# Kernel optimization log

Measured on AMD Instinct MI355X. Metric: run time of the kernel, lower is better.

## Reference

```python
import jax, jax.numpy as jnp
import numpy as np

B, N, E = 4, 2048, 1024
A, H = 64, 16          # attention_feature_dim, heads
D = A                   # per-head dim per source's rearrange quirk: d = attention_feature_dim
DK = A / H              # source scales by sqrt(attention_feature_dim / heads) = sqrt(4)
NEG_INF = jnp.float32(-jnp.inf)


def setup_inputs() -> dict:
    key = jax.random.key(0)
    ks = jax.random.split(key, 6)
    x = jax.random.normal(ks[0], (B, N, E), dtype=jnp.float32)
    mask = jax.random.randint(ks[1], (B, N), 0, 2, dtype=jnp.int32)
    # nn.Linear(E, A*H*3): weight [out,in] -> store transposed [in,out] for x @ W
    w_qkv = jax.random.normal(ks[2], (E, A * H * 3), dtype=jnp.float32) / np.sqrt(E)
    b_qkv = jax.random.normal(ks[3], (A * H * 3,), dtype=jnp.float32) * 0.02
    w_out = jax.random.normal(ks[4], (A * H, E), dtype=jnp.float32) / np.sqrt(A * H)
    b_out = jax.random.normal(ks[5], (E,), dtype=jnp.float32) * 0.02
    return {"x": x, "mask": mask, "w_qkv": w_qkv, "b_qkv": b_qkv,
            "w_out": w_out, "b_out": b_out}


def reference(x, mask, w_qkv, b_qkv, w_out, b_out):
    b, n, _ = x.shape
    qkv = x @ w_qkv + b_qkv                         # [b, n, 3*H*D]
    q, k, v = jnp.split(qkv, 3, axis=-1)            # each [b, n, H*D]
    def to_heads(t):
        return t.reshape(b, n, H, D).transpose(0, 2, 1, 3)  # [b, H, n, D]
    q, k, v = to_heads(q), to_heads(k), to_heads(v)
    scale = jnp.float32(1.0 / np.sqrt(DK))
    scores = jnp.einsum('bhqd,bhkd->bhqk', q, k) * scale    # [b, H, n, n]
    # mask: [b, n] -> [b, 1, 1, n]; masked positions (==0) get -inf
    scores = jnp.where(mask[:, None, None, :] == 0, NEG_INF, scores)
    attn = jax.nn.softmax(scores, axis=-1)
    out = jnp.einsum('bhqk,bhkd->bhqd', attn, v)            # [b, H, n, D]
    out = out.transpose(0, 2, 1, 3).reshape(b, n, H * D)    # [b, n, H*D]
    return out @ w_out + b_out                              # [b, n, E]
```

## Files before the change

kernel.cpp:

```cpp
#include <hip/hip_runtime.h>


typedef __bf16 bf16;
typedef __attribute__((ext_vector_type(8))) __bf16 bf16x8;
typedef __attribute__((ext_vector_type(4))) float f32x4;

#define MFMA16(a, b, c) __builtin_amdgcn_mfma_f32_16x16x32_bf16(a, b, c, 0, 0, 0)
#define GLOAD_LDS(src, dst) __builtin_amdgcn_global_load_lds( \
    (const __attribute__((address_space(1))) void*)(src),     \
    (__attribute__((address_space(3))) void*)(dst), 16, 0, 0)
#define BAR() __builtin_amdgcn_s_barrier()
#define VMCNT(n) asm volatile("s_waitcnt vmcnt(" #n ")" ::: "memory")

#define QSCALE 0.72134752f

__global__ __launch_bounds__(256, 1) void cvt_f32_bf16(
    const float* __restrict__ in, bf16* __restrict__ out, int n4)
{
    int i = blockIdx.x * 256 + threadIdx.x;
    if (i >= n4) return;
    float4 v = *(const float4*)(in + (size_t)i * 4);
    union { ushort4 u; bf16 h[4]; } o;
    o.h[0] = (bf16)v.x; o.h[1] = (bf16)v.y; o.h[2] = (bf16)v.z; o.h[3] = (bf16)v.w;
    *(ushort4*)(out + (size_t)i * 4) = o.u;
}

__global__ __launch_bounds__(256, 1) void transpose_f32_bf16(
    const float* __restrict__ in, bf16* __restrict__ out, int R, int C,
    int scale_rows, float scale)
{
    __shared__ float s[64][65];
    const int t  = threadIdx.x;
    const int r0 = blockIdx.y * 64;
    const int c0 = blockIdx.x * 64;
    const int tr  = t >> 4;
    const int tc4 = (t & 15) * 4;
#pragma unroll
    for (int p = 0; p < 4; ++p) {
        int r = tr + p * 16;
        float4 v = *(const float4*)(in + (size_t)(r0 + r) * C + c0 + tc4);
        s[r][tc4 + 0] = v.x; s[r][tc4 + 1] = v.y;
        s[r][tc4 + 2] = v.z; s[r][tc4 + 3] = v.w;
    }
    __syncthreads();
    const int cw  = t >> 3;
    const int rw8 = (t & 7) * 8;
#pragma unroll
    for (int p = 0; p < 2; ++p) {
        int c = cw + p * 32;
        float f = (c0 + c) < scale_rows ? scale : 1.0f;
        union { uint4 v; bf16 h[8]; } u;
#pragma unroll
        for (int j = 0; j < 8; ++j) u.h[j] = (bf16)(s[rw8 + j][c] * f);
        *(uint4*)(out + (size_t)(c0 + c) * R + r0 + rw8) = u.v;
    }
}

template <typename OutT>
__global__ __launch_bounds__(512, 2) void gemm128x256_kernel(
    const bf16* __restrict__ A, const bf16* __restrict__ Bt,
    const float* __restrict__ bias, OutT* __restrict__ C,
    int M, int N, int K, int qcols, float qscale, int nbx)
{
    __shared__ __align__(16) bf16 As[3 * 128 * 64];
    __shared__ __align__(16) bf16 Bs[3 * 256 * 64];

    const int t    = threadIdx.x;
    const int lane = t & 63;
    const int wave = t >> 6;
    const int wr   = wave >> 2;
    const int wc   = wave & 3;
    const int l15  = lane & 15;
    const int g    = lane >> 4;

    const int nwg = gridDim.x;
    const int cpx = nwg >> 3;
    const int wg  = blockIdx.x;
    const int swz = (wg & 7) * cpx + (wg >> 3);
    const int m0  = (swz / nbx) * 128;
    const int n0  = (swz % nbx) * 256;

    const int ntile = K >> 6;

    int srow[2], sblk[2];
#pragma unroll
    for (int r = 0; r < 2; ++r) {
        int s = t * 16 + r * 8192;
        srow[r] = s >> 7;
        int blk = (s >> 4) & 7;
        sblk[r] = blk ^ (srow[r] & 7);
    }
    const int ldst0 = t * 8;

    const bf16* Abase = A  + (size_t)m0 * K;
    const bf16* Bbase = Bt + (size_t)n0 * K;

    const f32x4 z = {0.f, 0.f, 0.f, 0.f};
    f32x4 acc[4][4];
#pragma unroll
    for (int i = 0; i < 4; ++i)
#pragma unroll
        for (int j = 0; j < 4; ++j) acc[i][j] = z;

    auto stageA = [&](int tile, int slot) {
        if (tile >= ntile) return;
        bf16* dst = As + slot * 8192;
        const bf16* src = Abase + tile * 64;
#pragma unroll
        for (int r = 0; r < 2; ++r)
            GLOAD_LDS(src + (size_t)srow[r] * K + sblk[r] * 8,
                      dst + ldst0 + r * 4096);
    };
    auto stageBh = [&](int tile, int slot, int h) {
        if (tile >= ntile) return;
        bf16* dst = Bs + slot * 16384 + h * 8192;
        const bf16* src = Bbase + (size_t)(h * 128) * K + tile * 64;
#pragma unroll
        for (int r = 0; r < 2; ++r)
            GLOAD_LDS(src + (size_t)srow[r] * K + sblk[r] * 8,
                      dst + ldst0 + r * 4096);
    };

#define LOAD_AF(slot)                                                         \
    _Pragma("unroll")                                                         \
    for (int f = 0; f < 4; ++f) {                                             \
        int row = wr * 64 + f * 16 + l15;                                     \
        _Pragma("unroll")                                                     \
        for (int ks = 0; ks < 2; ++ks)                                        \
            af[f][ks] = *(const bf16x8*)(&As[(slot) * 8192 + row * 64 +       \
                            (((ks * 4 + g) ^ (row & 7)) * 8)]);               \
    }
#define LOAD_BF(slot, half, dstv)                                             \
    _Pragma("unroll")                                                         \
    for (int c2 = 0; c2 < 2; ++c2) {                                          \
        int row = wc * 64 + ((half) * 2 + c2) * 16 + l15;                     \
        _Pragma("unroll")                                                     \
        for (int ks = 0; ks < 2; ++ks)                                        \
            dstv[c2][ks] = *(const bf16x8*)(&Bs[(slot) * 16384 + row * 64 +   \
                            (((ks * 4 + g) ^ (row & 7)) * 8)]);               \
    }
#define MFMA_H(bv, half)                                                      \
    {                                                                         \
        __builtin_amdgcn_s_setprio(1);                                        \
        _Pragma("unroll")                                                     \
        for (int f = 0; f < 4; ++f)                                           \
            _Pragma("unroll")                                                 \
            for (int c2 = 0; c2 < 2; ++c2) {                                  \
                acc[f][(half) * 2 + c2] = MFMA16(                             \
                    af[f][0], bv[c2][0], acc[f][(half) * 2 + c2]);            \
                acc[f][(half) * 2 + c2] = MFMA16(                             \
                    af[f][1], bv[c2][1], acc[f][(half) * 2 + c2]);            \
            }                                                                 \
        __builtin_amdgcn_s_setprio(0);                                        \
    }

    stageA(0, 0); stageBh(0, 0, 0); stageBh(0, 0, 1);
    stageA(1, 1); stageBh(1, 1, 0); stageBh(1, 1, 1);
    VMCNT(6);
    BAR();

    int slot = 0;
    for (int T = 0; T < ntile; ++T) {
        int slot2 = slot + 2; if (slot2 >= 3) slot2 -= 3;
        bf16x8 af[4][2], blo[2][2], bhi[2][2];
        LOAD_AF(slot);
        LOAD_BF(slot, 0, blo);
        stageA(T + 2, slot2);
        stageBh(T + 2, slot2, 0);
        MFMA_H(blo, 0);
        BAR();
        LOAD_BF(slot, 1, bhi);
        stageBh(T + 2, slot2, 1);
        MFMA_H(bhi, 1);
        if (T + 1 < ntile) {
            if (T + 2 < ntile) { VMCNT(6); } else { VMCNT(0); }
        }
        BAR();
        slot = (slot == 2) ? 0 : slot + 1;
    }

#undef LOAD_AF
#undef LOAD_BF
#undef MFMA_H

#pragma unroll
    for (int f = 0; f < 4; ++f) {
        int row = m0 + wr * 64 + f * 16 + g * 4;
#pragma unroll
        for (int cf = 0; cf < 4; ++cf) {
            int col = n0 + wc * 64 + cf * 16 + l15;
            float bs = bias[col];
            if (col < qcols) bs *= qscale;
#pragma unroll
            for (int r = 0; r < 4; ++r) {
                float v = acc[f][cf][r] + bs;
                C[(size_t)(row + r) * N + col] = (OutT)v;
            }
        }
    }
}

__global__ __launch_bounds__(256, 1) void vtrans_kernel(
    const bf16* __restrict__ qkv, bf16* __restrict__ vtg)
{
    __shared__ float tile[64][65];
    const int t  = threadIdx.x;
    const int n0 = blockIdx.x * 64;
    const int bh = blockIdx.y;
    const int b  = bh >> 4, h = bh & 15;
    const bf16* src = qkv + (size_t)(b * 2048 + n0) * 3072 + 2048 + h * 64;
#pragma unroll
    for (int r = 0; r < 2; ++r) {
        int s = t + r * 256;
        int row = s >> 3, c8 = (s & 7) * 8;
        union { uint4 v; bf16 h8[8]; } u;
        u.v = *(const uint4*)(src + (size_t)row * 3072 + c8);
#pragma unroll
        for (int j = 0; j < 8; ++j) tile[row][c8 + j] = (float)u.h8[j];
    }
    __syncthreads();
    bf16* dst = vtg + (size_t)bh * (64 * 2048) + n0;
#pragma unroll
    for (int r = 0; r < 2; ++r) {
        int s = t + r * 256;
        int d = s >> 3, n8 = (s & 7) * 8;
        union { uint4 v; bf16 h8[8]; } o;
#pragma unroll
        for (int j = 0; j < 8; ++j) o.h8[j] = (bf16)tile[n8 + j][d];
        *(uint4*)(dst + (size_t)d * 2048 + n8) = o.v;
    }
}

__global__ __launch_bounds__(256, 3) void attn_kernel(
    const bf16* __restrict__ qkv, const bf16* __restrict__ vtg,
    const int* __restrict__ mask, bf16* __restrict__ O)
{
    __shared__ __align__(16) bf16 Ks[2][64 * 64];
    __shared__ __align__(16) bf16 Vt[2][64 * 64];
    __shared__ __align__(16) bf16 Ps[4][16 * 88];
    __shared__ float mneg[2048];

    const int t    = threadIdx.x;
    const int lane = t & 63;
    const int wave = t >> 6;
    const int l15  = lane & 15;
    const int g    = lane >> 4;

    const int bid = (blockIdx.x & 7) * 128 + (blockIdx.x >> 3);
    const int qt  = bid & 15;
    const int bh  = bid >> 4;
    const int h   = bh & 15;
    const int b   = bh >> 4;
    const int q0  = qt * 128 + wave * 16;

    const int* mrow = mask + b * 2048;
    for (int i = t; i < 2048; i += 256)
        mneg[i] = mrow[i] ? 0.0f : -1e30f;

    const size_t RS = 3072;
    const bf16* qp0 = qkv + (size_t)(b * 2048 + q0 + l15) * RS + h * 64 + g * 8;
    const bf16* qp1 = qp0 + (size_t)64 * RS;
    bf16x8 aQ[2][2];
    aQ[0][0] = *(const bf16x8*)(qp0);
    aQ[0][1] = *(const bf16x8*)(qp0 + 32);
    aQ[1][0] = *(const bf16x8*)(qp1);
    aQ[1][1] = *(const bf16x8*)(qp1 + 32);

    const bf16* kbase = qkv + (size_t)(b * 2048) * RS + 1024 + h * 64;
    const bf16* vbase = vtg + (size_t)bh * (64 * 2048);

    const int e0 = t * 8;
    int srow[2], scol[2];
#pragma unroll
    for (int r = 0; r < 2; ++r) {
        int e   = e0 + r * 2048;
        int row = e >> 6;
        int cb  = (e >> 3) & 7;
        srow[r] = row;
        scol[r] = ((cb ^ (row & 7)) * 8);
    }

    const int rb0 = ((g)     ^ (l15 & 7)) * 8;
    const int rb1 = ((4 + g) ^ (l15 & 7)) * 8;

    const f32x4 z = {0.f, 0.f, 0.f, 0.f};
    f32x4 o0[4] = {z, z, z, z}, o1[4] = {z, z, z, z};
    f32x4 lacc0 = z, lacc1 = z;

    bf16x8 ones;
#pragma unroll
    for (int j = 0; j < 8; ++j) ones[j] = (bf16)1.0f;

#pragma unroll
    for (int r = 0; r < 2; ++r) {
        GLOAD_LDS(kbase + (size_t)srow[r] * RS + scol[r],   &Ks[0][e0 + r * 2048]);
        GLOAD_LDS(vbase + (size_t)srow[r] * 2048 + scol[r], &Vt[0][e0 + r * 2048]);
    }
    asm volatile("s_waitcnt vmcnt(0)" ::: "memory");
    __syncthreads();

    for (int i = 0; i < 32; ++i) {
        const int kc  = i * 64;
        const int buf = i & 1;

        if (i + 1 < 32) {
#pragma unroll
            for (int r = 0; r < 2; ++r) {
                GLOAD_LDS(kbase + (size_t)(kc + 64 + srow[r]) * RS + scol[r],
                          &Ks[buf ^ 1][e0 + r * 2048]);
                GLOAD_LDS(vbase + (size_t)srow[r] * 2048 + kc + 64 + scol[r],
                          &Vt[buf ^ 1][e0 + r * 2048]);
            }
        }

        float mb[4];
#pragma unroll
        for (int kt = 0; kt < 4; ++kt) mb[kt] = mneg[kc + kt * 16 + l15];

        bf16x8 bk[4][2];
#pragma unroll
        for (int kt = 0; kt < 4; ++kt) {
            const bf16* kr = &Ks[buf][(kt * 16 + l15) * 64];
            bk[kt][0] = *(const bf16x8*)(kr + rb0);
            bk[kt][1] = *(const bf16x8*)(kr + rb1);
        }

        f32x4 S[4];
#pragma unroll
        for (int kt = 0; kt < 4; ++kt) {
            f32x4 ini = {mb[kt], mb[kt], mb[kt], mb[kt]};
            S[kt] = MFMA16(aQ[0][0], bk[kt][0], ini);
            S[kt] = MFMA16(aQ[0][1], bk[kt][1], S[kt]);
        }
#pragma unroll
        for (int kt = 0; kt < 4; ++kt)
#pragma unroll
            for (int r = 0; r < 4; ++r)
                Ps[wave][(g * 4 + r) * 88 + kt * 16 + l15] =
                    (bf16)__builtin_amdgcn_exp2f(S[kt][r]);
        asm volatile("s_waitcnt lgkmcnt(0)" ::: "memory");
        const bf16x8 aP00 = *(const bf16x8*)(&Ps[wave][l15 * 88 + g * 8]);
        const bf16x8 aP01 = *(const bf16x8*)(&Ps[wave][l15 * 88 + 32 + g * 8]);
        asm volatile("s_waitcnt lgkmcnt(0)" ::: "memory");

#pragma unroll
        for (int kt = 0; kt < 4; ++kt) {
            f32x4 ini = {mb[kt], mb[kt], mb[kt], mb[kt]};
            S[kt] = MFMA16(aQ[1][0], bk[kt][0], ini);
            S[kt] = MFMA16(aQ[1][1], bk[kt][1], S[kt]);
        }

        bf16x8 bv[4][2];
#pragma unroll
        for (int dt = 0; dt < 4; ++dt) {
            const bf16* vr = &Vt[buf][(dt * 16 + l15) * 64];
            bv[dt][0] = *(const bf16x8*)(vr + rb0);
            bv[dt][1] = *(const bf16x8*)(vr + rb1);
        }

#pragma unroll
        for (int kt = 0; kt < 4; ++kt)
#pragma unroll
            for (int r = 0; r < 4; ++r)
                Ps[wave][(g * 4 + r) * 88 + kt * 16 + l15] =
                    (bf16)__builtin_amdgcn_exp2f(S[kt][r]);

        lacc0 = MFMA16(aP00, ones, lacc0);
        lacc0 = MFMA16(aP01, ones, lacc0);
#pragma unroll
        for (int dt = 0; dt < 4; ++dt) {
            o0[dt] = MFMA16(aP00, bv[dt][0], o0[dt]);
            o0[dt] = MFMA16(aP01, bv[dt][1], o0[dt]);
        }
        asm volatile("s_waitcnt lgkmcnt(0)" ::: "memory");
        const bf16x8 aP10 = *(const bf16x8*)(&Ps[wave][l15 * 88 + g * 8]);
        const bf16x8 aP11 = *(const bf16x8*)(&Ps[wave][l15 * 88 + 32 + g * 8]);

        lacc1 = MFMA16(aP10, ones, lacc1);
        lacc1 = MFMA16(aP11, ones, lacc1);
#pragma unroll
        for (int dt = 0; dt < 4; ++dt) {
            o1[dt] = MFMA16(aP10, bv[dt][0], o1[dt]);
            o1[dt] = MFMA16(aP11, bv[dt][1], o1[dt]);
        }

        asm volatile("s_waitcnt vmcnt(0)" ::: "memory");
        __syncthreads();
    }

    float inv0[4], inv1[4];
#pragma unroll
    for (int r = 0; r < 4; ++r) {
        inv0[r] = 1.0f / fmaxf(lacc0[r], 1e-30f);
        inv1[r] = 1.0f / fmaxf(lacc1[r], 1e-30f);
    }
#pragma unroll
    for (int nt = 0; nt < 4; ++nt) {
#pragma unroll
        for (int r = 0; r < 4; ++r) {
            int d = nt * 16 + l15;
            int row0 = q0 + g * 4 + r;
            O[(size_t)(b * 2048 + row0) * 1024 + h * 64 + d] = (bf16)(o0[nt][r] * inv0[r]);
            O[(size_t)(b * 2048 + row0 + 64) * 1024 + h * 64 + d] = (bf16)(o1[nt][r] * inv1[r]);
        }
    }
}

extern "C" void kernel_launch(void* const* d_in, const int* in_sizes, int n_in,
                              void* d_out, int out_size, void* d_ws, size_t ws_size,
                              hipStream_t stream)
{
    const float* x     = (const float*)d_in[0];
    const int*   mask  = (const int*)d_in[1];
    const float* w_qkv = (const float*)d_in[2];
    const float* b_qkv = (const float*)d_in[3];
    const float* w_out = (const float*)d_in[4];
    const float* b_out = (const float*)d_in[5];
    float* out = (float*)d_out;

    char* ws = (char*)d_ws;
    bf16* qkvb  = (bf16*)(ws);
    bf16* Obuf  = (bf16*)(ws + 50331648);
    bf16* xb    = (bf16*)(ws + 67108864);
    bf16* wqkvT = (bf16*)(ws + 83886080);
    bf16* woutT = (bf16*)(ws + 90177536);
    bf16* vtg   = xb;

    cvt_f32_bf16<<<dim3(8192), 256, 0, stream>>>(x, xb, 2097152);
    transpose_f32_bf16<<<dim3(48, 16), 256, 0, stream>>>(w_qkv, wqkvT, 1024, 3072,
                                                         1024, QSCALE);
    transpose_f32_bf16<<<dim3(16, 16), 256, 0, stream>>>(w_out, woutT, 1024, 1024,
                                                         0, 1.0f);
    gemm128x256_kernel<bf16><<<dim3(768), 512, 0, stream>>>(
        xb, wqkvT, b_qkv, qkvb, 8192, 3072, 1024, 1024, QSCALE, 12);
    vtrans_kernel<<<dim3(32, 64), 256, 0, stream>>>(qkvb, vtg);
    attn_kernel<<<dim3(1024), 256, 0, stream>>>(qkvb, vtg, mask, Obuf);
    gemm128x256_kernel<float><<<dim3(256), 512, 0, stream>>>(
        Obuf, woutT, b_out, out, 8192, 1024, 1024, 0, 1.0f, 4);
}
```

Before: 302.6 us.

## Compute transposed scores so P stays in registers, dropping the LDS round trip

Swaps the MFMA operand order so S^T comes out in a layout that can feed straight into the PV MFMA as the B operand. This removes the per-wave Ps shared-memory staging buffer and its waits. The row-sum MFMAs against a ones vector are replaced with scalar accumulation plus cross-lane swizzle and bpermute reductions at the end. V fragments are now read with split 8-byte LDS loads to match the new layout, and output stores are vectorized to 4 bf16 per store. The risks are more VGPR pressure, since both S tiles stay live, and more scalar adds in the softmax loop.

```diff
diff --git a/kernel.cpp b/kernel.cpp
--- a/kernel.cpp
+++ b/kernel.cpp
@@ -237,8 +237,7 @@
 {
     __shared__ __align__(16) bf16 Ks[2][64 * 64];
     __shared__ __align__(16) bf16 Vt[2][64 * 64];
-    __shared__ __align__(16) bf16 Ps[4][16 * 88];
-    __shared__ float mneg[2048];
+    __shared__ __align__(16) float mneg[2048];
 
     const int t    = threadIdx.x;
     const int lane = t & 63;
@@ -285,11 +284,7 @@
 
     const f32x4 z = {0.f, 0.f, 0.f, 0.f};
     f32x4 o0[4] = {z, z, z, z}, o1[4] = {z, z, z, z};
-    f32x4 lacc0 = z, lacc1 = z;
-
-    bf16x8 ones;
-#pragma unroll
-    for (int j = 0; j < 8; ++j) ones[j] = (bf16)1.0f;
+    float dsum0 = 0.0f, dsum1 = 0.0f;
 
 #pragma unroll
     for (int r = 0; r < 2; ++r) {
@@ -313,96 +308,80 @@
             }
         }
 
-        float mb[4];
-#pragma unroll
-        for (int kt = 0; kt < 4; ++kt) mb[kt] = mneg[kc + kt * 16 + l15];
-
-        bf16x8 bk[4][2];
+        f32x4 S0[4], S1[4];
 #pragma unroll
         for (int kt = 0; kt < 4; ++kt) {
+            f32x4 mq;
+#pragma unroll
+            for (int r = 0; r < 4; ++r)
+                mq[r] = mneg[kc + kt * 16 + g * 4 + r];
             const bf16* kr = &Ks[buf][(kt * 16 + l15) * 64];
-            bk[kt][0] = *(const bf16x8*)(kr + rb0);
-            bk[kt][1] = *(const bf16x8*)(kr + rb1);
-        }
-
-        f32x4 S[4];
-#pragma unroll
-        for (int kt = 0; kt < 4; ++kt) {
-            f32x4 ini = {mb[kt], mb[kt], mb[kt], mb[kt]};
-            S[kt] = MFMA16(aQ[0][0], bk[kt][0], ini);
-            S[kt] = MFMA16(aQ[0][1], bk[kt][1], S[kt]);
-        }
-#pragma unroll
-        for (int kt = 0; kt < 4; ++kt)
-#pragma unroll
-            for (int r = 0; r < 4; ++r)
-                Ps[wave][(g * 4 + r) * 88 + kt * 16 + l15] =
-                    (bf16)__builtin_amdgcn_exp2f(S[kt][r]);
-        asm volatile("s_waitcnt lgkmcnt(0)" ::: "memory");
-        const bf16x8 aP00 = *(const bf16x8*)(&Ps[wave][l15 * 88 + g * 8]);
-        const bf16x8 aP01 = *(const bf16x8*)(&Ps[wave][l15 * 88 + 32 + g * 8]);
-        asm volatile("s_waitcnt lgkmcnt(0)" ::: "memory");
-
-#pragma unroll
-        for (int kt = 0; kt < 4; ++kt) {
-            f32x4 ini = {mb[kt], mb[kt], mb[kt], mb[kt]};
-            S[kt] = MFMA16(aQ[1][0], bk[kt][0], ini);
-            S[kt] = MFMA16(aQ[1][1], bk[kt][1], S[kt]);
-        }
-
-        bf16x8 bv[4][2];
+            bf16x8 bk0 = *(const bf16x8*)(kr + rb0);
+            bf16x8 bk1 = *(const bf16x8*)(kr + rb1);
+            S0[kt] = MFMA16(bk0, aQ[0][0], mq);
+            S0[kt] = MFMA16(bk1, aQ[0][1], S0[kt]);
+            S1[kt] = MFMA16(bk0, aQ[1][0], mq);
+            S1[kt] = MFMA16(bk1, aQ[1][1], S1[kt]);
+        }
+
+        bf16x8 pb0[2], pb1[2];
+#pragma unroll
+        for (int m = 0; m < 2; ++m) {
+            union { bf16 hh[8]; bf16x8 v; } a, c;
+#pragma unroll
+            for (int kk = 0; kk < 2; ++kk) {
+#pragma unroll
+                for (int r = 0; r < 4; ++r) {
+                    float e0f = __builtin_amdgcn_exp2f(S0[2 * m + kk][r]);
+                    float e1f = __builtin_amdgcn_exp2f(S1[2 * m + kk][r]);
+                    a.hh[kk * 4 + r] = (bf16)e0f;
+                    c.hh[kk * 4 + r] = (bf16)e1f;
+                    dsum0 += e0f;
+                    dsum1 += e1f;
+                }
+            }
+            pb0[m] = a.v;
+            pb1[m] = c.v;
+        }
+
 #pragma unroll
         for (int dt = 0; dt < 4; ++dt) {
             const bf16* vr = &Vt[buf][(dt * 16 + l15) * 64];
-            bv[dt][0] = *(const bf16x8*)(vr + rb0);
-            bv[dt][1] = *(const bf16x8*)(vr + rb1);
-        }
-
-#pragma unroll
-        for (int kt = 0; kt < 4; ++kt)
-#pragma unroll
-            for (int r = 0; r < 4; ++r)
-                Ps[wave][(g * 4 + r) * 88 + kt * 16 + l15] =
-                    (bf16)__builtin_amdgcn_exp2f(S[kt][r]);
-
-        lacc0 = MFMA16(aP00, ones, lacc0);
-        lacc0 = MFMA16(aP01, ones, lacc0);
-#pragma unroll
-        for (int dt = 0; dt < 4; ++dt) {
-            o0[dt] = MFMA16(aP00, bv[dt][0], o0[dt]);
-            o0[dt] = MFMA16(aP01, bv[dt][1], o0[dt]);
-        }
-        asm volatile("s_waitcnt lgkmcnt(0)" ::: "memory");
-        const bf16x8 aP10 = *(const bf16x8*)(&Ps[wave][l15 * 88 + g * 8]);
-        const bf16x8 aP11 = *(const bf16x8*)(&Ps[wave][l15 * 88 + 32 + g * 8]);
-
-        lacc1 = MFMA16(aP10, ones, lacc1);
-        lacc1 = MFMA16(aP11, ones, lacc1);
-#pragma unroll
-        for (int dt = 0; dt < 4; ++dt) {
-            o1[dt] = MFMA16(aP10, bv[dt][0], o1[dt]);
-            o1[dt] = MFMA16(aP11, bv[dt][1], o1[dt]);
+            const int s7 = l15 & 7;
+#pragma unroll
+            for (int m = 0; m < 2; ++m) {
+                union { uint2 d2[2]; bf16x8 v; } vv;
+                vv.d2[0] = *(const uint2*)(vr + (((4 * m     + (g >> 1)) ^ s7) * 8) + (g & 1) * 4);
+                vv.d2[1] = *(const uint2*)(vr + (((4 * m + 2 + (g >> 1)) ^ s7) * 8) + (g & 1) * 4);
+                o0[dt] = MFMA16(vv.v, pb0[m], o0[dt]);
+                o1[dt] = MFMA16(vv.v, pb1[m], o1[dt]);
+            }
         }
 
         asm volatile("s_waitcnt vmcnt(0)" ::: "memory");
         __syncthreads();
     }
 
-    float inv0[4], inv1[4];
-#pragma unroll
-    for (int r = 0; r < 4; ++r) {
-        inv0[r] = 1.0f / fmaxf(lacc0[r], 1e-30f);
-        inv1[r] = 1.0f / fmaxf(lacc1[r], 1e-30f);
-    }
-#pragma unroll
-    for (int nt = 0; nt < 4; ++nt) {
+    dsum0 += __int_as_float(__builtin_amdgcn_ds_swizzle(__float_as_int(dsum0), 0x401F));
+    dsum1 += __int_as_float(__builtin_amdgcn_ds_swizzle(__float_as_int(dsum1), 0x401F));
+    const int swap32 = (lane ^ 32) << 2;
+    dsum0 += __int_as_float(__builtin_amdgcn_ds_bpermute(swap32, __float_as_int(dsum0)));
+    dsum1 += __int_as_float(__builtin_amdgcn_ds_bpermute(swap32, __float_as_int(dsum1)));
+    const float inv0 = 1.0f / fmaxf(dsum0, 1e-30f);
+    const float inv1 = 1.0f / fmaxf(dsum1, 1e-30f);
+
+    bf16* op0 = O + (size_t)(b * 2048 + q0 + l15) * 1024 + h * 64 + g * 4;
+    bf16* op1 = op0 + (size_t)64 * 1024;
+#pragma unroll
+    for (int dt = 0; dt < 4; ++dt) {
+        union { bf16 hh[4]; ushort4 u; } s0, s1;
 #pragma unroll
         for (int r = 0; r < 4; ++r) {
-            int d = nt * 16 + l15;
-            int row0 = q0 + g * 4 + r;
-            O[(size_t)(b * 2048 + row0) * 1024 + h * 64 + d] = (bf16)(o0[nt][r] * inv0[r]);
-            O[(size_t)(b * 2048 + row0 + 64) * 1024 + h * 64 + d] = (bf16)(o1[nt][r] * inv1[r]);
-        }
+            s0.hh[r] = (bf16)(o0[dt][r] * inv0);
+            s1.hh[r] = (bf16)(o1[dt][r] * inv1);
+        }
+        *(ushort4*)(op0 + dt * 16) = s0.u;
+        *(ushort4*)(op1 + dt * 16) = s1.u;
     }
 }
 
```

New measurement: 297.1 us. No clear change (-1.8%).
